# Optimization experiments

Hardware: AMD Instinct MI355X
Metric: run time of the kernel (lower is better)

## Reference

```python
import jax, jax.numpy as jnp
import numpy as np

IMG_SIZE = 640


def _decode_level(cls, box, img_size):
    """cls: [B,C,H,W] logits, box: [B,4,H,W] offsets -> ([B,HW,4], [B,HW,1], [B,HW])."""
    B = cls.shape[0]
    cls = jnp.transpose(cls, (0, 2, 3, 1))          # [B,H,W,C]
    box = jnp.transpose(box, (0, 2, 3, 1))          # [B,H,W,4]
    prob = jax.nn.sigmoid(cls)
    conf = jnp.max(prob, axis=-1, keepdims=True)    # [B,H,W,1]
    cidx = jnp.argmax(prob, axis=-1)                # [B,H,W]
    stage = box.shape[1]                            # H (== W)
    step = img_size // stage                        # stride for this level
    grid = jnp.arange(stage, dtype=box.dtype) * step
    gx, gy = jnp.meshgrid(grid, grid, indexing='xy')
    block = jnp.stack([gx, gy], axis=-1)            # [H,W,2] anchor-point coords
    tl = block - box[..., :2]                       # x1,y1
    br = block + box[..., 2:4]                      # x2,y2
    boxes = jnp.concatenate([tl, br], axis=-1).reshape(B, -1, 4)
    scores = conf.reshape(B, -1, 1)
    classes = cidx.reshape(B, -1).astype(jnp.int64)
    return boxes, scores, classes


def setup_inputs() -> dict:
    key = jax.random.key(0)
    ks = jax.random.split(key, 6)
    return {
        'cls0': jax.random.normal(ks[0], (64, 80, 80, 80), dtype=jnp.float32),
        'box0': jax.random.uniform(ks[1], (64, 4, 80, 80), dtype=jnp.float32) * 32.0,
        'cls1': jax.random.normal(ks[2], (64, 80, 40, 40), dtype=jnp.float32),
        'box1': jax.random.uniform(ks[3], (64, 4, 40, 40), dtype=jnp.float32) * 64.0,
        'cls2': jax.random.normal(ks[4], (64, 80, 20, 20), dtype=jnp.float32),
        'box2': jax.random.uniform(ks[5], (64, 4, 20, 20), dtype=jnp.float32) * 128.0,
    }


def reference(cls0, box0, cls1, box1, cls2, box2):
    levels = [(cls0, box0), (cls1, box1), (cls2, box2)]
    boxes_l, scores_l, classes_l = [], [], []
    for cls, box in levels:
        b, s, c = _decode_level(cls, box, IMG_SIZE)
        boxes_l.append(b)
        scores_l.append(s)
        classes_l.append(c)
    boxes = jnp.concatenate(boxes_l, axis=1)      # [B,N,4]
    scores = jnp.concatenate(scores_l, axis=1)    # [B,N,1]
    classes = jnp.concatenate(classes_l, axis=1)  # [B,N]
    boxes = jnp.clip(boxes, 0.0, IMG_SIZE - 1)
    return boxes, scores, classes
```

## Files before the change

### kernel.cpp

```cpp
#include <hip/hip_runtime.h>
#include <cmath>


constexpr int B_   = 64;
constexpr int NC   = 80;
constexpr int NTOT = 8400;

template<int HW, int W, int STEP, int NOFF>
__device__ __forceinline__ void decode_level(
    const float* __restrict__ cls, const float* __restrict__ box,
    float* __restrict__ oboxes, float* __restrict__ oscores, float* __restrict__ oclasses,
    int lbid, int tid)
{
    constexpr int QPI = HW / 4;

    int t  = lbid * 256 + tid;
    int b  = t / QPI;
    int p  = (t - b * QPI) << 2;

    const float* cbase = cls + (size_t)b * NC * HW + p;
    float m[4]  = {-3.4e38f, -3.4e38f, -3.4e38f, -3.4e38f};
    int   ci[4] = {0, 0, 0, 0};
    #pragma unroll 8
    for (int c = 0; c < NC; ++c) {
        float4 v = *reinterpret_cast<const float4*>(cbase + (size_t)c * HW);
        float vv[4] = {v.x, v.y, v.z, v.w};
        #pragma unroll
        for (int j = 0; j < 4; ++j) {
            if (vv[j] > m[j]) { m[j] = vv[j]; ci[j] = c; }
        }
    }

    size_t obase = (size_t)b * NTOT + NOFF + p;
    float4 osc, ocl;
    osc.x = 1.0f / (1.0f + __expf(-m[0]));
    osc.y = 1.0f / (1.0f + __expf(-m[1]));
    osc.z = 1.0f / (1.0f + __expf(-m[2]));
    osc.w = 1.0f / (1.0f + __expf(-m[3]));
    ocl.x = (float)ci[0]; ocl.y = (float)ci[1]; ocl.z = (float)ci[2]; ocl.w = (float)ci[3];
    *reinterpret_cast<float4*>(oscores  + obase) = osc;
    *reinterpret_cast<float4*>(oclasses + obase) = ocl;

    int base = lbid * 1024;
    #pragma unroll
    for (int k = 0; k < 4; ++k) {
        int P  = base + tid + (k << 8);
        int bb = P / HW;
        int pp = P - bb * HW;
        int hh = pp / W;
        int ww = pp - hh * W;

        const float* bbase = box + (size_t)bb * 4 * HW + pp;
        float l  = bbase[0];
        float tt = bbase[HW];
        float r  = bbase[2 * HW];
        float dd = bbase[3 * HW];

        float gx = (float)(ww * STEP);
        float gy = (float)(hh * STEP);
        float4 o;
        o.x = fminf(fmaxf(gx - l,  0.0f), 639.0f);
        o.y = fminf(fmaxf(gy - tt, 0.0f), 639.0f);
        o.z = fminf(fmaxf(gx + r,  0.0f), 639.0f);
        o.w = fminf(fmaxf(gy + dd, 0.0f), 639.0f);

        size_t ob = (size_t)bb * NTOT + NOFF + pp;
        *reinterpret_cast<float4*>(oboxes + ob * 4) = o;
    }
}

__global__ __launch_bounds__(256) void rtmdet_decode_fused(
    const float* __restrict__ cls0, const float* __restrict__ box0,
    const float* __restrict__ cls1, const float* __restrict__ box1,
    const float* __restrict__ cls2, const float* __restrict__ box2,
    float* __restrict__ oboxes, float* __restrict__ oscores, float* __restrict__ oclasses)
{
    int bid = blockIdx.x;
    int tid = threadIdx.x;
    if (bid < 400) {
        decode_level<6400, 80,  8,    0>(cls0, box0, oboxes, oscores, oclasses, bid,       tid);
    } else if (bid < 500) {
        decode_level<1600, 40, 16, 6400>(cls1, box1, oboxes, oscores, oclasses, bid - 400, tid);
    } else {
        decode_level< 400, 20, 32, 8000>(cls2, box2, oboxes, oscores, oclasses, bid - 500, tid);
    }
}

extern "C" void kernel_launch(void* const* d_in, const int* in_sizes, int n_in,
                              void* d_out, int out_size, void* d_ws, size_t ws_size,
                              hipStream_t stream) {
    const float* cls0 = (const float*)d_in[0];
    const float* box0 = (const float*)d_in[1];
    const float* cls1 = (const float*)d_in[2];
    const float* box1 = (const float*)d_in[3];
    const float* cls2 = (const float*)d_in[4];
    const float* box2 = (const float*)d_in[5];

    float* oboxes   = (float*)d_out;
    float* oscores  = oboxes  + (size_t)B_ * NTOT * 4;
    float* oclasses = oscores + (size_t)B_ * NTOT;

    rtmdet_decode_fused<<<525, 256, 0, stream>>>(cls0, box0, cls1, box1, cls2, box2,
                                                 oboxes, oscores, oclasses);
}
```

Measured before the change: 35.09 us.

## Split class reduction across four lanes with shuffle-based argmax merge

Each group of four adjacent threads now splits the 80-class max/argmax for a quad of pixels into four 20-class chunks. The partial results are combined with xor shuffles, breaking ties toward the lower class index. The grid grows fourfold and each thread handles one box instead of four. This raises parallelism and the number of loads in flight for the bandwidth-bound class read, at the cost of shuffle work and narrower scalar score and class stores.

```diff
diff --git a/kernel.cpp b/kernel.cpp
--- a/kernel.cpp
+++ b/kernel.cpp
@@ -5,6 +5,8 @@
 constexpr int B_   = 64;
 constexpr int NC   = 80;
 constexpr int NTOT = 8400;
+
+__device__ __forceinline__ float sigmoidf_(float x) { return 1.0f / (1.0f + __expf(-x)); }
 
 template<int HW, int W, int STEP, int NOFF>
 __device__ __forceinline__ void decode_level(
@@ -14,15 +16,17 @@
 {
     constexpr int QPI = HW / 4;
 
-    int t  = lbid * 256 + tid;
-    int b  = t / QPI;
-    int p  = (t - b * QPI) << 2;
+    int gt    = lbid * 256 + tid;
+    int quad  = gt >> 2;
+    int chunk = gt & 3;
+    int b     = quad / QPI;
+    int p     = (quad - b * QPI) << 2;
 
-    const float* cbase = cls + (size_t)b * NC * HW + p;
+    const float* cbase = cls + (size_t)b * NC * HW + (size_t)(chunk * 20) * HW + p;
     float m[4]  = {-3.4e38f, -3.4e38f, -3.4e38f, -3.4e38f};
     int   ci[4] = {0, 0, 0, 0};
-    #pragma unroll 8
-    for (int c = 0; c < NC; ++c) {
+    #pragma unroll
+    for (int c = 0; c < 20; ++c) {
         float4 v = *reinterpret_cast<const float4*>(cbase + (size_t)c * HW);
         float vv[4] = {v.x, v.y, v.z, v.w};
         #pragma unroll
@@ -30,21 +34,26 @@
             if (vv[j] > m[j]) { m[j] = vv[j]; ci[j] = c; }
         }
     }
+    int cofs = chunk * 20;
+    #pragma unroll
+    for (int j = 0; j < 4; ++j) ci[j] += cofs;
 
-    size_t obase = (size_t)b * NTOT + NOFF + p;
-    float4 osc, ocl;
-    osc.x = 1.0f / (1.0f + __expf(-m[0]));
-    osc.y = 1.0f / (1.0f + __expf(-m[1]));
-    osc.z = 1.0f / (1.0f + __expf(-m[2]));
-    osc.w = 1.0f / (1.0f + __expf(-m[3]));
-    ocl.x = (float)ci[0]; ocl.y = (float)ci[1]; ocl.z = (float)ci[2]; ocl.w = (float)ci[3];
-    *reinterpret_cast<float4*>(oscores  + obase) = osc;
-    *reinterpret_cast<float4*>(oclasses + obase) = ocl;
+    #pragma unroll
+    for (int mask = 1; mask <= 2; mask <<= 1) {
+        #pragma unroll
+        for (int j = 0; j < 4; ++j) {
+            float om = __shfl_xor(m[j],  mask);
+            int   oc = __shfl_xor(ci[j], mask);
+            if (om > m[j] || (om == m[j] && oc < ci[j])) { m[j] = om; ci[j] = oc; }
+        }
+    }
 
-    int base = lbid * 1024;
-    #pragma unroll
-    for (int k = 0; k < 4; ++k) {
-        int P  = base + tid + (k << 8);
+    size_t obase = (size_t)b * NTOT + NOFF + p + chunk;
+    oscores [obase] = sigmoidf_(m[chunk]);
+    oclasses[obase] = (float)ci[chunk];
+
+    {
+        int P  = lbid * 256 + tid;
         int bb = P / HW;
         int pp = P - bb * HW;
         int hh = pp / W;
@@ -77,12 +86,12 @@
 {
     int bid = blockIdx.x;
     int tid = threadIdx.x;
-    if (bid < 400) {
-        decode_level<6400, 80,  8,    0>(cls0, box0, oboxes, oscores, oclasses, bid,       tid);
-    } else if (bid < 500) {
-        decode_level<1600, 40, 16, 6400>(cls1, box1, oboxes, oscores, oclasses, bid - 400, tid);
+    if (bid < 1600) {
+        decode_level<6400, 80,  8,    0>(cls0, box0, oboxes, oscores, oclasses, bid,        tid);
+    } else if (bid < 2000) {
+        decode_level<1600, 40, 16, 6400>(cls1, box1, oboxes, oscores, oclasses, bid - 1600, tid);
     } else {
-        decode_level< 400, 20, 32, 8000>(cls2, box2, oboxes, oscores, oclasses, bid - 500, tid);
+        decode_level< 400, 20, 32, 8000>(cls2, box2, oboxes, oscores, oclasses, bid - 2000, tid);
     }
 }
 
@@ -100,6 +109,6 @@
     float* oscores  = oboxes  + (size_t)B_ * NTOT * 4;
     float* oclasses = oscores + (size_t)B_ * NTOT;
 
-    rtmdet_decode_fused<<<525, 256, 0, stream>>>(cls0, box0, cls1, box1, cls2, box2,
-                                                 oboxes, oscores, oclasses);
+    rtmdet_decode_fused<<<2100, 256, 0, stream>>>(cls0, box0, cls1, box1, cls2, box2,
+                                                  oboxes, oscores, oclasses);
 }
```

After: 48.41 us. +38.0%, slower.

## Process two pixels per thread and double grid for more parallelism

Applied to the files above, without the earlier changes.

Each thread now handles two adjacent pixels instead of four, using float2 loads across the 80 class channels. The launch grid doubles to 1050 blocks to raise occupancy and memory-level parallelism. Box decoding is remapped so each thread decodes the same pixels it scores, loading box offsets as float2. Narrower loads may lower per-request efficiency.

```diff
diff --git a/kernel.cpp b/kernel.cpp
--- a/kernel.cpp
+++ b/kernel.cpp
@@ -6,66 +6,56 @@
 constexpr int NC   = 80;
 constexpr int NTOT = 8400;
 
+__device__ __forceinline__ float sigmoidf_(float x) { return 1.0f / (1.0f + __expf(-x)); }
+
 template<int HW, int W, int STEP, int NOFF>
 __device__ __forceinline__ void decode_level(
     const float* __restrict__ cls, const float* __restrict__ box,
     float* __restrict__ oboxes, float* __restrict__ oscores, float* __restrict__ oclasses,
     int lbid, int tid)
 {
-    constexpr int QPI = HW / 4;
+    constexpr int PPI = HW / 2;
 
-    int t  = lbid * 256 + tid;
-    int b  = t / QPI;
-    int p  = (t - b * QPI) << 2;
+    int t = lbid * 256 + tid;
+    int b = t / PPI;
+    int p = (t - b * PPI) << 1;
+    int h = p / W;
+    int w = p - h * W;
+
+    const float* bbase = box + (size_t)b * 4 * HW + p;
+    float2 bl = *reinterpret_cast<const float2*>(bbase);
+    float2 bt = *reinterpret_cast<const float2*>(bbase + HW);
+    float2 br = *reinterpret_cast<const float2*>(bbase + 2 * HW);
+    float2 bd = *reinterpret_cast<const float2*>(bbase + 3 * HW);
 
     const float* cbase = cls + (size_t)b * NC * HW + p;
-    float m[4]  = {-3.4e38f, -3.4e38f, -3.4e38f, -3.4e38f};
-    int   ci[4] = {0, 0, 0, 0};
-    #pragma unroll 8
+    float m[2]  = {-3.4e38f, -3.4e38f};
+    int   ci[2] = {0, 0};
+    #pragma unroll 16
     for (int c = 0; c < NC; ++c) {
-        float4 v = *reinterpret_cast<const float4*>(cbase + (size_t)c * HW);
-        float vv[4] = {v.x, v.y, v.z, v.w};
-        #pragma unroll
-        for (int j = 0; j < 4; ++j) {
-            if (vv[j] > m[j]) { m[j] = vv[j]; ci[j] = c; }
-        }
+        float2 v = *reinterpret_cast<const float2*>(cbase + (size_t)c * HW);
+        if (v.x > m[0]) { m[0] = v.x; ci[0] = c; }
+        if (v.y > m[1]) { m[1] = v.y; ci[1] = c; }
     }
 
     size_t obase = (size_t)b * NTOT + NOFF + p;
-    float4 osc, ocl;
-    osc.x = 1.0f / (1.0f + __expf(-m[0]));
-    osc.y = 1.0f / (1.0f + __expf(-m[1]));
-    osc.z = 1.0f / (1.0f + __expf(-m[2]));
-    osc.w = 1.0f / (1.0f + __expf(-m[3]));
-    ocl.x = (float)ci[0]; ocl.y = (float)ci[1]; ocl.z = (float)ci[2]; ocl.w = (float)ci[3];
-    *reinterpret_cast<float4*>(oscores  + obase) = osc;
-    *reinterpret_cast<float4*>(oclasses + obase) = ocl;
+    *reinterpret_cast<float2*>(oscores  + obase) = make_float2(sigmoidf_(m[0]), sigmoidf_(m[1]));
+    *reinterpret_cast<float2*>(oclasses + obase) = make_float2((float)ci[0], (float)ci[1]);
 
-    int base = lbid * 1024;
+    float gy = (float)(h * STEP);
     #pragma unroll
-    for (int k = 0; k < 4; ++k) {
-        int P  = base + tid + (k << 8);
-        int bb = P / HW;
-        int pp = P - bb * HW;
-        int hh = pp / W;
-        int ww = pp - hh * W;
-
-        const float* bbase = box + (size_t)bb * 4 * HW + pp;
-        float l  = bbase[0];
-        float tt = bbase[HW];
-        float r  = bbase[2 * HW];
-        float dd = bbase[3 * HW];
-
-        float gx = (float)(ww * STEP);
-        float gy = (float)(hh * STEP);
+    for (int j = 0; j < 2; ++j) {
+        float gx = (float)((w + j) * STEP);
+        float l  = j ? bl.y : bl.x;
+        float tt = j ? bt.y : bt.x;
+        float r  = j ? br.y : br.x;
+        float dd = j ? bd.y : bd.x;
         float4 o;
         o.x = fminf(fmaxf(gx - l,  0.0f), 639.0f);
         o.y = fminf(fmaxf(gy - tt, 0.0f), 639.0f);
         o.z = fminf(fmaxf(gx + r,  0.0f), 639.0f);
         o.w = fminf(fmaxf(gy + dd, 0.0f), 639.0f);
-
-        size_t ob = (size_t)bb * NTOT + NOFF + pp;
-        *reinterpret_cast<float4*>(oboxes + ob * 4) = o;
+        *reinterpret_cast<float4*>(oboxes + (obase + j) * 4) = o;
     }
 }
 
@@ -77,12 +67,12 @@
 {
     int bid = blockIdx.x;
     int tid = threadIdx.x;
-    if (bid < 400) {
-        decode_level<6400, 80,  8,    0>(cls0, box0, oboxes, oscores, oclasses, bid,       tid);
-    } else if (bid < 500) {
-        decode_level<1600, 40, 16, 6400>(cls1, box1, oboxes, oscores, oclasses, bid - 400, tid);
+    if (bid < 800) {
+        decode_level<6400, 80,  8,    0>(cls0, box0, oboxes, oscores, oclasses, bid,        tid);
+    } else if (bid < 1000) {
+        decode_level<1600, 40, 16, 6400>(cls1, box1, oboxes, oscores, oclasses, bid - 800,  tid);
     } else {
-        decode_level< 400, 20, 32, 8000>(cls2, box2, oboxes, oscores, oclasses, bid - 500, tid);
+        decode_level< 400, 20, 32, 8000>(cls2, box2, oboxes, oscores, oclasses, bid - 1000, tid);
     }
 }
 
@@ -100,6 +90,6 @@
     float* oscores  = oboxes  + (size_t)B_ * NTOT * 4;
     float* oclasses = oscores + (size_t)B_ * NTOT;
 
-    rtmdet_decode_fused<<<525, 256, 0, stream>>>(cls0, box0, cls1, box1, cls2, box2,
-                                                 oboxes, oscores, oclasses);
+    rtmdet_decode_fused<<<1050, 256, 0, stream>>>(cls0, box0, cls1, box1, cls2, box2,
+                                                  oboxes, oscores, oclasses);
 }
```

Result: faster. 33.67 us (median of 2 runs) (-4.0%).

## Stream class logits through LDS with async global_load_lds multi-stage pipeline

Applied to the files above, without the earlier changes.

Replaces the direct per-thread float4 loop over 80 class channels with a 4-stage software pipeline. It uses global_load_lds to prefetch 4-channel chunks into 64KB of shared memory and gates each stage with explicit s_waitcnt vmcnt counts. Box decoding now reads float2 pairs and handles two pixels per iteration. The aim is more memory-level parallelism for this bandwidth-bound kernel. In exchange, the large LDS footprint cuts occupancy, and the hand-written waitcnt values depend on the compiler issuing no other vector memory ops in between.

```diff
diff --git a/kernel.cpp b/kernel.cpp
--- a/kernel.cpp
+++ b/kernel.cpp
@@ -6,66 +6,109 @@
 constexpr int NC   = 80;
 constexpr int NTOT = 8400;
 
+typedef float f32x4 __attribute__((ext_vector_type(4)));
+
+__device__ __forceinline__ float sigmoidf_(float x) { return 1.0f / (1.0f + __expf(-x)); }
+
+__device__ __forceinline__ void gld16(const void* g, void* l) {
+    __builtin_amdgcn_global_load_lds(
+        (const __attribute__((address_space(1))) void*)g,
+        (__attribute__((address_space(3))) void*)l, 16, 0, 0);
+}
+
 template<int HW, int W, int STEP, int NOFF>
 __device__ __forceinline__ void decode_level(
     const float* __restrict__ cls, const float* __restrict__ box,
     float* __restrict__ oboxes, float* __restrict__ oscores, float* __restrict__ oclasses,
-    int lbid, int tid)
+    int lbid, int tid, f32x4* __restrict__ sb )
 {
     constexpr int QPI = HW / 4;
+    constexpr int PPI = HW / 2;
 
-    int t  = lbid * 256 + tid;
-    int b  = t / QPI;
-    int p  = (t - b * QPI) << 2;
+    int Q = lbid * 256 + tid;
+    int b = Q / QPI;
+    int p = (Q - b * QPI) << 2;
 
-    const float* cbase = cls + (size_t)b * NC * HW + p;
+    const float* gsrc = cls + (size_t)b * NC * HW + p;
+
     float m[4]  = {-3.4e38f, -3.4e38f, -3.4e38f, -3.4e38f};
     int   ci[4] = {0, 0, 0, 0};
-    #pragma unroll 8
-    for (int c = 0; c < NC; ++c) {
-        float4 v = *reinterpret_cast<const float4*>(cbase + (size_t)c * HW);
-        float vv[4] = {v.x, v.y, v.z, v.w};
-        #pragma unroll
-        for (int j = 0; j < 4; ++j) {
-            if (vv[j] > m[j]) { m[j] = vv[j]; ci[j] = c; }
-        }
+
+#define STAGE(ch) {                                                        \
+        const float* s_ = gsrc + (size_t)(ch) * 4 * HW;                    \
+        f32x4* d_ = sb + ((ch) & 3) * 1024 + tid;                          \
+        gld16(s_,            d_);                                          \
+        gld16(s_ +     HW,   d_ + 256);                                    \
+        gld16(s_ + 2 * HW,   d_ + 512);                                    \
+        gld16(s_ + 3 * HW,   d_ + 768);                                    \
     }
+
+#define RED1(v, c) {                                                       \
+        if (v.x > m[0]) { m[0] = v.x; ci[0] = (c); }                       \
+        if (v.y > m[1]) { m[1] = v.y; ci[1] = (c); }                       \
+        if (v.z > m[2]) { m[2] = v.z; ci[2] = (c); }                       \
+        if (v.w > m[3]) { m[3] = v.w; ci[3] = (c); }                       \
+    }
+
+#define CHUNK(i, WN) {                                                     \
+        asm volatile("s_waitcnt vmcnt(" #WN ")" ::: "memory");             \
+        const f32x4* bp = sb + ((i) & 3) * 1024 + tid;                     \
+        f32x4 v0 = bp[0], v1 = bp[256], v2 = bp[512], v3 = bp[768];        \
+        RED1(v0, (i) * 4 + 0) RED1(v1, (i) * 4 + 1)                        \
+        RED1(v2, (i) * 4 + 2) RED1(v3, (i) * 4 + 3)                        \
+        if ((i) + 4 < 20) STAGE((i) + 4)                                   \
+    }
+
+    STAGE(0) STAGE(1) STAGE(2) STAGE(3)
+
+    CHUNK( 0, 12) CHUNK( 1, 12) CHUNK( 2, 12) CHUNK( 3, 12)
+    CHUNK( 4, 12) CHUNK( 5, 12) CHUNK( 6, 12) CHUNK( 7, 12)
+    CHUNK( 8, 12) CHUNK( 9, 12) CHUNK(10, 12) CHUNK(11, 12)
+    CHUNK(12, 12) CHUNK(13, 12) CHUNK(14, 12) CHUNK(15, 12)
+    CHUNK(16, 12) CHUNK(17,  8) CHUNK(18,  4) CHUNK(19,  0)
+
+#undef STAGE
+#undef RED1
+#undef CHUNK
 
     size_t obase = (size_t)b * NTOT + NOFF + p;
     float4 osc, ocl;
-    osc.x = 1.0f / (1.0f + __expf(-m[0]));
-    osc.y = 1.0f / (1.0f + __expf(-m[1]));
-    osc.z = 1.0f / (1.0f + __expf(-m[2]));
-    osc.w = 1.0f / (1.0f + __expf(-m[3]));
+    osc.x = sigmoidf_(m[0]); osc.y = sigmoidf_(m[1]);
+    osc.z = sigmoidf_(m[2]); osc.w = sigmoidf_(m[3]);
     ocl.x = (float)ci[0]; ocl.y = (float)ci[1]; ocl.z = (float)ci[2]; ocl.w = (float)ci[3];
     *reinterpret_cast<float4*>(oscores  + obase) = osc;
     *reinterpret_cast<float4*>(oclasses + obase) = ocl;
 
-    int base = lbid * 1024;
     #pragma unroll
-    for (int k = 0; k < 4; ++k) {
-        int P  = base + tid + (k << 8);
-        int bb = P / HW;
-        int pp = P - bb * HW;
+    for (int s = 0; s < 2; ++s) {
+        int PR = lbid * 512 + tid + (s << 8);
+        int bb = PR / PPI;
+        int pp = (PR - bb * PPI) << 1;
         int hh = pp / W;
         int ww = pp - hh * W;
 
         const float* bbase = box + (size_t)bb * 4 * HW + pp;
-        float l  = bbase[0];
-        float tt = bbase[HW];
-        float r  = bbase[2 * HW];
-        float dd = bbase[3 * HW];
+        float2 bl = *reinterpret_cast<const float2*>(bbase);
+        float2 bt = *reinterpret_cast<const float2*>(bbase + HW);
+        float2 br = *reinterpret_cast<const float2*>(bbase + 2 * HW);
+        float2 bd = *reinterpret_cast<const float2*>(bbase + 3 * HW);
 
-        float gx = (float)(ww * STEP);
         float gy = (float)(hh * STEP);
-        float4 o;
-        o.x = fminf(fmaxf(gx - l,  0.0f), 639.0f);
-        o.y = fminf(fmaxf(gy - tt, 0.0f), 639.0f);
-        o.z = fminf(fmaxf(gx + r,  0.0f), 639.0f);
-        o.w = fminf(fmaxf(gy + dd, 0.0f), 639.0f);
-
         size_t ob = (size_t)bb * NTOT + NOFF + pp;
-        *reinterpret_cast<float4*>(oboxes + ob * 4) = o;
+        #pragma unroll
+        for (int j = 0; j < 2; ++j) {
+            float gx = (float)((ww + j) * STEP);
+            float l  = j ? bl.y : bl.x;
+            float tt = j ? bt.y : bt.x;
+            float r  = j ? br.y : br.x;
+            float dd = j ? bd.y : bd.x;
+            float4 o;
+            o.x = fminf(fmaxf(gx - l,  0.0f), 639.0f);
+            o.y = fminf(fmaxf(gy - tt, 0.0f), 639.0f);
+            o.z = fminf(fmaxf(gx + r,  0.0f), 639.0f);
+            o.w = fminf(fmaxf(gy + dd, 0.0f), 639.0f);
+            *reinterpret_cast<float4*>(oboxes + (ob + j) * 4) = o;
+        }
     }
 }
 
@@ -75,14 +118,16 @@
     const float* __restrict__ cls2, const float* __restrict__ box2,
     float* __restrict__ oboxes, float* __restrict__ oscores, float* __restrict__ oclasses)
 {
+    __shared__ f32x4 sb[4 * 1024];
+
     int bid = blockIdx.x;
     int tid = threadIdx.x;
     if (bid < 400) {
-        decode_level<6400, 80,  8,    0>(cls0, box0, oboxes, oscores, oclasses, bid,       tid);
+        decode_level<6400, 80,  8,    0>(cls0, box0, oboxes, oscores, oclasses, bid,       tid, sb);
     } else if (bid < 500) {
-        decode_level<1600, 40, 16, 6400>(cls1, box1, oboxes, oscores, oclasses, bid - 400, tid);
+        decode_level<1600, 40, 16, 6400>(cls1, box1, oboxes, oscores, oclasses, bid - 400, tid, sb);
     } else {
-        decode_level< 400, 20, 32, 8000>(cls2, box2, oboxes, oscores, oclasses, bid - 500, tid);
+        decode_level< 400, 20, 32, 8000>(cls2, box2, oboxes, oscores, oclasses, bid - 500, tid, sb);
     }
 }
 
```

Result: slower. 40.85 us (+16.4%).
